# Optimization experiments

Hardware: AMD Instinct MI355X
Metric: run time of the kernel (lower is better)

## Reference

```python
import jax, jax.numpy as jnp
import numpy as np

NUM_BUCKETS = 64
MAX_DISTANCE = 50000.0


def setup_inputs() -> dict:
    R, I, N, E, H = 64, 512, 4, 256, 8
    key = jax.random.key(0)
    ks = jax.random.split(key, 12)
    p = lambda k, shape: (jax.random.normal(k, shape, dtype=jnp.float32) * 0.02)
    return {
        "x": jax.random.normal(ks[0], (R, I, N, E), dtype=jnp.float32),
        "distances": jax.random.randint(ks[1], (N, I, I), 0, 50000).astype(jnp.int32),
        "Wq": p(ks[2], (E, E)), "bq": jnp.zeros((E,), jnp.float32),
        "Wk": p(ks[3], (E, E)), "bk": jnp.zeros((E,), jnp.float32),
        "Wv": p(ks[4], (E, E)), "bv": jnp.zeros((E,), jnp.float32),
        "Wo": p(ks[5], (E, E)), "bo": jnp.zeros((E,), jnp.float32),
        "rel_emb": p(ks[6], (NUM_BUCKETS, H)),
    }


def reference(x, distances, Wq, bq, Wk, bk, Wv, bv, Wo, bo, rel_emb):
    R, I, N, E = x.shape
    H = rel_emb.shape[1]
    D = E // H
    # scaling = head_dim**-0.5 / sqrt(num_rows)
    scaling = (D ** -0.5) / np.sqrt(R)

    def proj(W, b):
        return (jnp.einsum('rine,fe->rinf', x, W) + b).reshape(R, I, N, H, D)

    q = proj(Wq, bq) * scaling
    k = proj(Wk, bk)
    v = proj(Wv, bv)

    # Row-summed attention logits: (H, N, I, J)
    attn_weights = jnp.einsum('rinhd,rjnhd->hnij', q, k)

    # T5-style relative position bias (buckets = linspace boundaries)
    buckets = jnp.linspace(0.0, MAX_DISTANCE, NUM_BUCKETS - 1)
    abs_dist = jnp.abs(distances).astype(jnp.float32)
    # torch.bucketize(right=False) == searchsorted side='left'
    bucket_idx = jnp.searchsorted(buckets, abs_dist, side='left')  # (N, I, J)
    bias = rel_emb[bucket_idx]                  # (N, I, J, H)
    attn_weights = attn_weights + jnp.transpose(bias, (3, 0, 1, 2))

    attn_probs = jax.nn.softmax(attn_weights, axis=-1)  # dropout p=0.0 -> identity

    context = jnp.einsum('hnij,rjnhd->rinhd', attn_probs, v).reshape(R, I, N, E)
    output = jnp.einsum('rine,fe->rinf', context, Wo) + bo
    return output, attn_probs
```

## Files before the change

kernel.cpp:

```cpp
#include <hip/hip_runtime.h>

typedef unsigned short u16;
typedef unsigned int u32;
typedef float f32x4 __attribute__((ext_vector_type(4)));
typedef short bf16x8 __attribute__((ext_vector_type(8)));
typedef unsigned short u16x8 __attribute__((ext_vector_type(8)));

#define SL 33554432u

__device__ __forceinline__ float bf2f(u16 u) {
  u32 v = ((u32)u) << 16;
  return __builtin_bit_cast(float, v);
}
__device__ __forceinline__ u16 f2bf(float f) {
  u32 i = __builtin_bit_cast(u32, f);
  i += 0x7fffu + ((i >> 16) & 1u);
  return (u16)(i >> 16);
}

#define GLDS16(g, l) __builtin_amdgcn_global_load_lds( \
    (const __attribute__((address_space(1))) void*)(g), \
    (__attribute__((address_space(3))) void*)(l), 16, 0, 0)

__device__ __forceinline__ void stage128(const u16* gbase, int ldk, u16* lds, int tid) {
  #pragma unroll
  for (int rep = 0; rep < 4; ++rep) {
    int c = tid + rep * 256;
    int row = c >> 3, slot = c & 7;
    const u16* g = gbase + (size_t)row * ldk + ((slot ^ (row & 7)) << 3);
    GLDS16(g, lds + c * 8);
  }
}

__device__ __forceinline__ void stage128_f32(const float* gbase, int ldk, u16* lds, int tid) {
  #pragma unroll
  for (int rep = 0; rep < 4; ++rep) {
    int c = tid + rep * 256;
    int row = c >> 3, slot = c & 7;
    const float* g = gbase + (size_t)row * ldk + ((slot ^ (row & 7)) << 3);
    float4 a = *(const float4*)g, b = *(const float4*)(g + 4);
    u16x8 o;
    o[0] = f2bf(a.x); o[1] = f2bf(a.y); o[2] = f2bf(a.z); o[3] = f2bf(a.w);
    o[4] = f2bf(b.x); o[5] = f2bf(b.y); o[6] = f2bf(b.z); o[7] = f2bf(b.w);
    *(u16x8*)(lds + c * 8) = o;
  }
}

__device__ __forceinline__ void mfma128(const u16* As, const u16* Bs, int lane,
                                        int wm0, int wn0, f32x4 acc[4][4]) {
  #pragma unroll
  for (int kk = 0; kk < 2; ++kk) {
    bf16x8 a[4], b[4];
    #pragma unroll
    for (int mi = 0; mi < 4; ++mi) {
      int r = wm0 + mi * 16 + (lane & 15);
      int c16 = (kk * 4 + (lane >> 4)) ^ (r & 7);
      a[mi] = *(const bf16x8*)(As + r * 64 + c16 * 8);
    }
    #pragma unroll
    for (int ni = 0; ni < 4; ++ni) {
      int r = wn0 + ni * 16 + (lane & 15);
      int c16 = (kk * 4 + (lane >> 4)) ^ (r & 7);
      b[ni] = *(const bf16x8*)(Bs + r * 64 + c16 * 8);
    }
    #pragma unroll
    for (int mi = 0; mi < 4; ++mi)
      #pragma unroll
      for (int ni = 0; ni < 4; ++ni)
        acc[mi][ni] = __builtin_amdgcn_mfma_f32_16x16x32_bf16(a[mi], b[ni], acc[mi][ni], 0, 0, 0);
  }
}

__device__ __forceinline__ void gemm_core(const u16* A, int ldkA, const u16* B, int ldkB,
                                          int NT, u16* As, u16* Bs,
                                          int tid, int lane, int wm0, int wn0,
                                          f32x4 acc[4][4]) {
  for (int t = 0; t < NT; ++t) {
    stage128(A + t * 64, ldkA, As, tid);
    stage128(B + t * 64, ldkB, Bs, tid);
    __syncthreads();
    mfma128(As, Bs, lane, wm0, wn0, acc);
    __syncthreads();
  }
}

__global__ __launch_bounds__(256) void k_castw(
    const float* __restrict__ Wq, const float* __restrict__ Wk,
    const float* __restrict__ Wv, const float* __restrict__ Wo,
    u16* __restrict__ Wb) {
  int idx = blockIdx.x * 256 + threadIdx.x;
  int w = idx >> 13, off = idx & 8191;
  const float* src = (w == 0) ? Wq : (w == 1) ? Wk : (w == 2) ? Wv : Wo;
  const float4* s = (const float4*)(src + (size_t)off * 8);
  float4 a = s[0], b = s[1];
  u16x8 o;
  o[0] = f2bf(a.x); o[1] = f2bf(a.y); o[2] = f2bf(a.z); o[3] = f2bf(a.w);
  o[4] = f2bf(b.x); o[5] = f2bf(b.y); o[6] = f2bf(b.z); o[7] = f2bf(b.w);
  *(u16x8*)(Wb + (size_t)w * 65536 + (size_t)off * 8) = o;
}

__global__ __launch_bounds__(256) void k_proj_mm(
    const float* __restrict__ x, const u16* __restrict__ Wb,
    const float* __restrict__ bq, const float* __restrict__ bk, const float* __restrict__ bv,
    u16* __restrict__ qt, u16* __restrict__ kt, u16* __restrict__ vt, float scaling) {
  __shared__ __align__(16) u16 As[128 * 64];
  __shared__ __align__(16) u16 Bs[128 * 64];
  const int tid = threadIdx.x, lane = tid & 63, wave = tid >> 6;
  const int wm0 = (wave >> 1) * 64, wn0 = (wave & 1) * 64;
  const int bid = blockIdx.x;
  const int sb = (bid & 7) * 768 + (bid >> 3);
  const int mt = sb / 6, g = sb % 6;
  const int m0 = mt * 128, n0 = (g & 1) * 128, w = g >> 1;

  f32x4 acc[4][4];
  #pragma unroll
  for (int mi = 0; mi < 4; ++mi)
    #pragma unroll
    for (int ni = 0; ni < 4; ++ni) acc[mi][ni] = (f32x4){0.f, 0.f, 0.f, 0.f};

  const float* Ax = x + (size_t)m0 * 256;
  const u16* Bw = Wb + w * 65536 + (size_t)n0 * 256;
  for (int t = 0; t < 4; ++t) {
    stage128_f32(Ax + t * 64, 256, As, tid);
    stage128(Bw + t * 64, 256, Bs, tid);
    __syncthreads();
    mfma128(As, Bs, lane, wm0, wn0, acc);
    __syncthreads();
  }

  const float* bias = (w == 0) ? bq : (w == 1) ? bk : bv;
  u16* dst = (w == 0) ? qt : (w == 1) ? kt : vt;
  const float sc = (w == 0) ? scaling : 1.0f;

  #pragma unroll
  for (int mi = 0; mi < 4; ++mi)
    #pragma unroll
    for (int ni = 0; ni < 4; ++ni) {
      int f = n0 + wn0 + ni * 16 + (lane & 15);
      int h = f >> 5, d = f & 31;
      float bb = bias[f];
      #pragma unroll
      for (int q = 0; q < 4; ++q) {
        int m = m0 + wm0 + mi * 16 + (lane >> 4) * 4 + q;
        int n = m & 3, i = (m >> 2) & 511, r = m >> 11;
        size_t o = ((size_t)((n * 8 + h) * 512 + i)) * 2048 + r * 32 + d;
        dst[o] = f2bf((acc[mi][ni][q] + bb) * sc);
      }
    }
}

__global__ __launch_bounds__(256) void k_attn_mm(
    const u16* __restrict__ qt, const u16* __restrict__ kt, u16* __restrict__ lgt) {
  __shared__ __align__(16) u16 As[128 * 64];
  __shared__ __align__(16) u16 Bs[128 * 64];
  const int tid = threadIdx.x, lane = tid & 63, wave = tid >> 6;
  const int wm0 = (wave >> 1) * 64, wn0 = (wave & 1) * 64;
  const int bid = blockIdx.x;
  const int sb = (bid & 7) * 64 + (bid >> 3);
  const int nh = sb >> 4, tt = sb & 15;
  const int m0 = (tt >> 2) * 128, n0 = (tt & 3) * 128;

  f32x4 acc[4][4];
  #pragma unroll
  for (int mi = 0; mi < 4; ++mi)
    #pragma unroll
    for (int ni = 0; ni < 4; ++ni) acc[mi][ni] = (f32x4){0.f, 0.f, 0.f, 0.f};

  const size_t base = (size_t)nh * 512 * 2048;
  gemm_core(qt + base + (size_t)m0 * 2048, 2048, kt + base + (size_t)n0 * 2048, 2048,
            32, As, Bs, tid, lane, wm0, wn0, acc);

  #pragma unroll
  for (int mi = 0; mi < 4; ++mi)
    #pragma unroll
    for (int ni = 0; ni < 4; ++ni) {
      int col = n0 + wn0 + ni * 16 + (lane & 15);
      #pragma unroll
      for (int q = 0; q < 4; ++q) {
        int row = m0 + wm0 + mi * 16 + (lane >> 4) * 4 + q;
        lgt[(size_t)nh * 262144 + (size_t)row * 512 + col] = f2bf(acc[mi][ni][q]);
      }
    }
}

__global__ __launch_bounds__(256) void k_softmax(
    const u16* __restrict__ lgt, const int* __restrict__ dist, const float* __restrict__ rel,
    float* __restrict__ probs, u16* __restrict__ pbf) {
  const int t = threadIdx.x;
  const int lane = t & 63, wv = t >> 6;
  const int b = blockIdx.x;
  const int i = b & 511, n = b >> 9;

  const int* dr = dist + ((size_t)n * 512 + i) * 512 + lane * 8;
  int4 dA = *(const int4*)dr, dB = *(const int4*)(dr + 4);
  int dd[8] = {dA.x, dA.y, dA.z, dA.w, dB.x, dB.y, dB.z, dB.w};
  int u[8];
  #pragma unroll
  for (int j = 0; j < 8; ++j) {
    int v = dd[j] < 0 ? -dd[j] : dd[j];
    int q = (62 * v + 49999) / 50000; if (q > 63) q = 63;
    u[j] = q;
  }

  #pragma unroll
  for (int hh = 0; hh < 2; ++hh) {
    const int h = wv * 2 + hh;
    const int nh = n * 8 + h;
    const u16* lr = lgt + ((size_t)nh * 512 + i) * 512 + lane * 8;
    u16x8 L = *(const u16x8*)lr;
    float vj[8];
    float mx = -1e30f;
    #pragma unroll
    for (int j = 0; j < 8; ++j) {
      vj[j] = bf2f(L[j]) + rel[u[j] * 8 + h];
      mx = fmaxf(mx, vj[j]);
    }
    #pragma unroll
    for (int off = 32; off; off >>= 1) mx = fmaxf(mx, __shfl_xor(mx, off));
    float s = 0.f;
    #pragma unroll
    for (int j = 0; j < 8; ++j) { vj[j] = __expf(vj[j] - mx); s += vj[j]; }
    #pragma unroll
    for (int off = 32; off; off >>= 1) s += __shfl_xor(s, off);
    float inv = 1.0f / s;
    float4 pa, pb;
    pa.x = vj[0]*inv; pa.y = vj[1]*inv; pa.z = vj[2]*inv; pa.w = vj[3]*inv;
    pb.x = vj[4]*inv; pb.y = vj[5]*inv; pb.z = vj[6]*inv; pb.w = vj[7]*inv;
    size_t po = ((size_t)(h * 4 + n) * 512 + i) * 512 + lane * 8;
    *(float4*)(probs + po) = pa;
    *(float4*)(probs + po + 4) = pb;
    u16x8 pc;
    pc[0]=f2bf(pa.x); pc[1]=f2bf(pa.y); pc[2]=f2bf(pa.z); pc[3]=f2bf(pa.w);
    pc[4]=f2bf(pb.x); pc[5]=f2bf(pb.y); pc[6]=f2bf(pb.z); pc[7]=f2bf(pb.w);
    size_t pq = ((size_t)nh * 512 + i) * 512 + lane * 8;
    *(u16x8*)(pbf + pq) = pc;
  }
}

__global__ __launch_bounds__(256) void k_vtrans(const u16* __restrict__ vt, u16* __restrict__ vtt) {
  __shared__ u16 ts[64][72];
  const int b = blockIdx.x;
  const int ct_ = b & 31, it = (b >> 5) & 7, nh = b >> 8;
  const int i0 = it * 64, c0 = ct_ * 64;
  const int t = threadIdx.x;
  #pragma unroll
  for (int rep = 0; rep < 2; ++rep) {
    int c = t + rep * 256;
    int r = c >> 3, q = c & 7;
    u16x8 v = *(const u16x8*)(vt + ((size_t)nh * 512 + i0 + r) * 2048 + c0 + q * 8);
    #pragma unroll
    for (int j = 0; j < 8; ++j) ts[r][q * 8 + j] = v[j];
  }
  __syncthreads();
  #pragma unroll
  for (int rep = 0; rep < 2; ++rep) {
    int c = t + rep * 256;
    int rr = c >> 3, q = c & 7;
    u16x8 o;
    #pragma unroll
    for (int j = 0; j < 8; ++j) o[j] = ts[q * 8 + j][rr];
    *(u16x8*)(vtt + ((size_t)nh * 2048 + c0 + rr) * 512 + i0 + q * 8) = o;
  }
}

__global__ __launch_bounds__(256) void k_ctx_mm(
    const u16* __restrict__ vtt, const u16* __restrict__ pbf, u16* __restrict__ ctT) {
  __shared__ __align__(16) u16 As[128 * 64];
  __shared__ __align__(16) u16 Bs[128 * 64];
  const int tid = threadIdx.x, lane = tid & 63, wave = tid >> 6;
  const int wm0 = (wave >> 1) * 64, wn0 = (wave & 1) * 64;
  const int bid = blockIdx.x;
  const int sb = (bid & 7) * 256 + (bid >> 3);
  const int nh = sb >> 6, tt = sb & 63;
  const int m0 = (tt >> 2) * 128, n0 = (tt & 3) * 128;

  f32x4 acc[4][4];
  #pragma unroll
  for (int mi = 0; mi < 4; ++mi)
    #pragma unroll
    for (int ni = 0; ni < 4; ++ni) acc[mi][ni] = (f32x4){0.f, 0.f, 0.f, 0.f};

  gemm_core(vtt + (size_t)nh * 1048576 + (size_t)m0 * 512, 512,
            pbf + (size_t)nh * 262144 + (size_t)n0 * 512, 512,
            8, As, Bs, tid, lane, wm0, wn0, acc);

  #pragma unroll
  for (int mi = 0; mi < 4; ++mi)
    #pragma unroll
    for (int ni = 0; ni < 4; ++ni) {
      int col = n0 + wn0 + ni * 16 + (lane & 15);
      #pragma unroll
      for (int q = 0; q < 4; ++q) {
        int row = m0 + wm0 + mi * 16 + (lane >> 4) * 4 + q;
        ctT[(size_t)nh * 1048576 + (size_t)row * 512 + col] = f2bf(acc[mi][ni][q]);
      }
    }
}

__global__ __launch_bounds__(256) void k_ctrans(const u16* __restrict__ ctT, u16* __restrict__ ct) {
  __shared__ u16 ts[32][520];
  const int b = blockIdx.x;
  const int r = b & 63, nh = b >> 6;
  const int n = nh >> 3, h = nh & 7;
  const int t = threadIdx.x;
  #pragma unroll
  for (int rep = 0; rep < 8; ++rep) {
    int c = t + rep * 256;
    int d = c >> 6, q = c & 63;
    u16x8 v = *(const u16x8*)(ctT + ((size_t)nh * 2048 + r * 32 + d) * 512 + q * 8);
    #pragma unroll
    for (int j = 0; j < 8; ++j) ts[d][q * 8 + j] = v[j];
  }
  __syncthreads();
  #pragma unroll
  for (int rep = 0; rep < 8; ++rep) {
    int c = t + rep * 256;
    int i = c >> 2, q = c & 3;
    u16x8 o;
    #pragma unroll
    for (int j = 0; j < 8; ++j) o[j] = ts[q * 8 + j][i];
    *(u16x8*)(ct + ((size_t)((r * 512 + i) * 4 + n)) * 256 + h * 32 + q * 8) = o;
  }
}

__global__ __launch_bounds__(256) void k_oproj_mm(
    const u16* __restrict__ ct, const u16* __restrict__ Wob,
    const float* __restrict__ bo, float* __restrict__ out) {
  __shared__ __align__(16) u16 As[128 * 64];
  __shared__ __align__(16) u16 Bs[128 * 64];
  const int tid = threadIdx.x, lane = tid & 63, wave = tid >> 6;
  const int wm0 = (wave >> 1) * 64, wn0 = (wave & 1) * 64;
  const int bid = blockIdx.x;
  const int sb = (bid & 7) * 256 + (bid >> 3);
  const int m0 = (sb >> 1) * 128, n0 = (sb & 1) * 128;

  f32x4 acc[4][4];
  #pragma unroll
  for (int mi = 0; mi < 4; ++mi)
    #pragma unroll
    for (int ni = 0; ni < 4; ++ni) acc[mi][ni] = (f32x4){0.f, 0.f, 0.f, 0.f};

  gemm_core(ct + (size_t)m0 * 256, 256, Wob + (size_t)n0 * 256, 256,
            4, As, Bs, tid, lane, wm0, wn0, acc);

  #pragma unroll
  for (int mi = 0; mi < 4; ++mi)
    #pragma unroll
    for (int ni = 0; ni < 4; ++ni) {
      int col = n0 + wn0 + ni * 16 + (lane & 15);
      float bb = bo[col];
      #pragma unroll
      for (int q = 0; q < 4; ++q) {
        int row = m0 + wm0 + mi * 16 + (lane >> 4) * 4 + q;
        out[(size_t)row * 256 + col] = acc[mi][ni][q] + bb;
      }
    }
}

extern "C" void kernel_launch(void* const* d_in, const int* in_sizes, int n_in,
                              void* d_out, int out_size, void* d_ws, size_t ws_size,
                              hipStream_t stream) {
  const float* x  = (const float*)d_in[0];
  const int* dist = (const int*)d_in[1];
  const float* Wq = (const float*)d_in[2];
  const float* bq = (const float*)d_in[3];
  const float* Wk = (const float*)d_in[4];
  const float* bk = (const float*)d_in[5];
  const float* Wv = (const float*)d_in[6];
  const float* bv = (const float*)d_in[7];
  const float* Wo = (const float*)d_in[8];
  const float* bo = (const float*)d_in[9];
  const float* rel = (const float*)d_in[10];
  float* out = (float*)d_out;
  float* probs = out + (size_t)SL;

  u16* ws = (u16*)d_ws;
  u16* lgt = ws;
  u16* qt  = ws + (size_t)SL;
  u16* kt  = ws + (size_t)2 * SL;
  u16* vt  = ws + (size_t)3 * SL;
  u16* pbf = qt;
  u16* vtt = kt;
  u16* ctT = vt;
  u16* ctb = lgt;
  u16* Wb  = ws + (size_t)4 * SL;

  const float scaling = 0.022097086912079608f;

  k_castw  <<<128, 256, 0, stream>>>(Wq, Wk, Wv, Wo, Wb);
  k_proj_mm<<<6144, 256, 0, stream>>>(x, Wb, bq, bk, bv, qt, kt, vt, scaling);
  k_attn_mm<<<512, 256, 0, stream>>>(qt, kt, lgt);
  k_softmax<<<2048, 256, 0, stream>>>(lgt, dist, rel, probs, pbf);
  k_vtrans <<<8192, 256, 0, stream>>>(vt, vtt);
  k_ctx_mm <<<2048, 256, 0, stream>>>(vtt, pbf, ctT);
  k_ctrans <<<2048, 256, 0, stream>>>(ctT, ctb);
  k_oproj_mm<<<2048, 256, 0, stream>>>(ctb, Wb + 196608, bo, out);
}
```

Before: 402.0 us.

## Fuse V and context transposes into GEMM epilogues; precast x to bf16

Removes the standalone k_vtrans and k_ctrans kernels. The projection and context GEMM epilogues now stage their tiles through LDS and write directly in the transposed layouts, using vectorized 16-byte stores instead of scattered 2-byte stores. x is converted to bf16 once by a separate cast kernel, so the projection GEMM can stage it with global_load_lds instead of per-thread fp32 loads and converts. This adds an extra full pass over x and a bf16 copy of it, and makes the epilogues more complex with possible LDS bank conflicts on the transposed V writes.

Result: faster. 374.8 us (-6.8%).

```diff
diff --git a/kernel.cpp b/kernel.cpp
--- a/kernel.cpp
+++ b/kernel.cpp
@@ -29,20 +29,6 @@
     int row = c >> 3, slot = c & 7;
     const u16* g = gbase + (size_t)row * ldk + ((slot ^ (row & 7)) << 3);
     GLDS16(g, lds + c * 8);
-  }
-}
-
-__device__ __forceinline__ void stage128_f32(const float* gbase, int ldk, u16* lds, int tid) {
-  #pragma unroll
-  for (int rep = 0; rep < 4; ++rep) {
-    int c = tid + rep * 256;
-    int row = c >> 3, slot = c & 7;
-    const float* g = gbase + (size_t)row * ldk + ((slot ^ (row & 7)) << 3);
-    float4 a = *(const float4*)g, b = *(const float4*)(g + 4);
-    u16x8 o;
-    o[0] = f2bf(a.x); o[1] = f2bf(a.y); o[2] = f2bf(a.z); o[3] = f2bf(a.w);
-    o[4] = f2bf(b.x); o[5] = f2bf(b.y); o[6] = f2bf(b.z); o[7] = f2bf(b.w);
-    *(u16x8*)(lds + c * 8) = o;
   }
 }
 
@@ -82,6 +68,17 @@
     mfma128(As, Bs, lane, wm0, wn0, acc);
     __syncthreads();
   }
+}
+
+__global__ __launch_bounds__(256) void k_castx(const float* __restrict__ src,
+                                               u16* __restrict__ dst) {
+  int idx = blockIdx.x * 256 + threadIdx.x;
+  const float4* s = (const float4*)src;
+  float4 a = s[(size_t)idx * 2], b = s[(size_t)idx * 2 + 1];
+  u16x8 o;
+  o[0] = f2bf(a.x); o[1] = f2bf(a.y); o[2] = f2bf(a.z); o[3] = f2bf(a.w);
+  o[4] = f2bf(b.x); o[5] = f2bf(b.y); o[6] = f2bf(b.z); o[7] = f2bf(b.w);
+  *(u16x8*)(dst + (size_t)idx * 8) = o;
 }
 
 __global__ __launch_bounds__(256) void k_castw(
@@ -100,17 +97,22 @@
 }
 
 __global__ __launch_bounds__(256) void k_proj_mm(
-    const float* __restrict__ x, const u16* __restrict__ Wb,
+    const u16* __restrict__ xb, const u16* __restrict__ Wb,
     const float* __restrict__ bq, const float* __restrict__ bk, const float* __restrict__ bv,
-    u16* __restrict__ qt, u16* __restrict__ kt, u16* __restrict__ vt, float scaling) {
-  __shared__ __align__(16) u16 As[128 * 64];
-  __shared__ __align__(16) u16 Bs[128 * 64];
+    u16* __restrict__ qt, u16* __restrict__ kt, u16* __restrict__ vtt, float scaling) {
+  __shared__ __align__(16) u16 lds[17408];
+  u16* As = lds;
+  u16* Bs = lds + 8192;
+  u16* ts = lds;
   const int tid = threadIdx.x, lane = tid & 63, wave = tid >> 6;
   const int wm0 = (wave >> 1) * 64, wn0 = (wave & 1) * 64;
   const int bid = blockIdx.x;
   const int sb = (bid & 7) * 768 + (bid >> 3);
   const int mt = sb / 6, g = sb % 6;
   const int m0 = mt * 128, n0 = (g & 1) * 128, w = g >> 1;
+  const int h0 = n0 >> 5;
+  const int r = mt >> 4;
+  const int i0 = (mt * 32) & 511;
 
   f32x4 acc[4][4];
   #pragma unroll
@@ -118,35 +120,68 @@
     #pragma unroll
     for (int ni = 0; ni < 4; ++ni) acc[mi][ni] = (f32x4){0.f, 0.f, 0.f, 0.f};
 
-  const float* Ax = x + (size_t)m0 * 256;
-  const u16* Bw = Wb + w * 65536 + (size_t)n0 * 256;
-  for (int t = 0; t < 4; ++t) {
-    stage128_f32(Ax + t * 64, 256, As, tid);
-    stage128(Bw + t * 64, 256, Bs, tid);
+  gemm_core(xb + (size_t)m0 * 256, 256, Wb + w * 65536 + (size_t)n0 * 256, 256,
+            4, As, Bs, tid, lane, wm0, wn0, acc);
+
+  const float* bias = (w == 0) ? bq : (w == 1) ? bk : bv;
+  const float sc = (w == 0) ? scaling : 1.0f;
+
+  if (w < 2) {
+    #pragma unroll
+    for (int mi = 0; mi < 4; ++mi)
+      #pragma unroll
+      for (int ni = 0; ni < 4; ++ni) {
+        int f_l = wn0 + ni * 16 + (lane & 15);
+        float bb = bias[n0 + f_l];
+        #pragma unroll
+        for (int q = 0; q < 4; ++q) {
+          int m_l = wm0 + mi * 16 + (lane >> 4) * 4 + q;
+          ts[m_l * 136 + f_l] = f2bf((acc[mi][ni][q] + bb) * sc);
+        }
+      }
     __syncthreads();
-    mfma128(As, Bs, lane, wm0, wn0, acc);
+    u16* dst = (w == 0) ? qt : kt;
+    #pragma unroll
+    for (int cc = 0; cc < 2; ++cc) {
+      int ch = tid + cc * 256;
+      int i_l = ch & 31, hh = (ch >> 5) & 3, n = ch >> 7;
+      const u16* src = ts + (i_l * 4 + n) * 136 + hh * 32;
+      size_t o = ((size_t)((n * 8 + h0 + hh) * 512) + i0 + i_l) * 2048 + r * 32;
+      #pragma unroll
+      for (int j = 0; j < 4; ++j)
+        *(u16x8*)(dst + o + j * 8) = *(const u16x8*)(src + j * 8);
+    }
+  } else {
+    #pragma unroll
+    for (int mi = 0; mi < 4; ++mi)
+      #pragma unroll
+      for (int ni = 0; ni < 4; ++ni) {
+        int f_l = wn0 + ni * 16 + (lane & 15);
+        float bb = bias[n0 + f_l];
+        #pragma unroll
+        for (int q = 0; q < 4; ++q) {
+          int m_l = wm0 + mi * 16 + (lane >> 4) * 4 + q;
+          ts[f_l * 136 + m_l] = f2bf(acc[mi][ni][q] + bb);
+        }
+      }
     __syncthreads();
-  }
-
-  const float* bias = (w == 0) ? bq : (w == 1) ? bk : bv;
-  u16* dst = (w == 0) ? qt : (w == 1) ? kt : vt;
-  const float sc = (w == 0) ? scaling : 1.0f;
-
-  #pragma unroll
-  for (int mi = 0; mi < 4; ++mi)
-    #pragma unroll
-    for (int ni = 0; ni < 4; ++ni) {
-      int f = n0 + wn0 + ni * 16 + (lane & 15);
-      int h = f >> 5, d = f & 31;
-      float bb = bias[f];
-      #pragma unroll
-      for (int q = 0; q < 4; ++q) {
-        int m = m0 + wm0 + mi * 16 + (lane >> 4) * 4 + q;
-        int n = m & 3, i = (m >> 2) & 511, r = m >> 11;
-        size_t o = ((size_t)((n * 8 + h) * 512 + i)) * 2048 + r * 32 + d;
-        dst[o] = f2bf((acc[mi][ni][q] + bb) * sc);
-      }
-    }
+    #pragma unroll
+    for (int cc = 0; cc < 2; ++cc) {
+      int ch = tid + cc * 256;
+      int d = ch & 31, hh = (ch >> 5) & 3, n = ch >> 7;
+      const u16* src = ts + (hh * 32 + d) * 136;
+      u16x8 tmp[4];
+      #pragma unroll
+      for (int j = 0; j < 4; ++j)
+        #pragma unroll
+        for (int e = 0; e < 8; ++e)
+          tmp[j][e] = src[(j * 8 + e) * 4 + n];
+      size_t o = ((size_t)(n * 8 + h0 + hh) * 2048 + r * 32 + d) * 512 + i0;
+      #pragma unroll
+      for (int j = 0; j < 4; ++j)
+        *(u16x8*)(vtt + o + j * 8) = tmp[j];
+    }
+  }
 }
 
 __global__ __launch_bounds__(256) void k_attn_mm(
@@ -237,42 +272,19 @@
   }
 }
 
-__global__ __launch_bounds__(256) void k_vtrans(const u16* __restrict__ vt, u16* __restrict__ vtt) {
-  __shared__ u16 ts[64][72];
-  const int b = blockIdx.x;
-  const int ct_ = b & 31, it = (b >> 5) & 7, nh = b >> 8;
-  const int i0 = it * 64, c0 = ct_ * 64;
-  const int t = threadIdx.x;
-  #pragma unroll
-  for (int rep = 0; rep < 2; ++rep) {
-    int c = t + rep * 256;
-    int r = c >> 3, q = c & 7;
-    u16x8 v = *(const u16x8*)(vt + ((size_t)nh * 512 + i0 + r) * 2048 + c0 + q * 8);
-    #pragma unroll
-    for (int j = 0; j < 8; ++j) ts[r][q * 8 + j] = v[j];
-  }
-  __syncthreads();
-  #pragma unroll
-  for (int rep = 0; rep < 2; ++rep) {
-    int c = t + rep * 256;
-    int rr = c >> 3, q = c & 7;
-    u16x8 o;
-    #pragma unroll
-    for (int j = 0; j < 8; ++j) o[j] = ts[q * 8 + j][rr];
-    *(u16x8*)(vtt + ((size_t)nh * 2048 + c0 + rr) * 512 + i0 + q * 8) = o;
-  }
-}
-
 __global__ __launch_bounds__(256) void k_ctx_mm(
-    const u16* __restrict__ vtt, const u16* __restrict__ pbf, u16* __restrict__ ctT) {
-  __shared__ __align__(16) u16 As[128 * 64];
-  __shared__ __align__(16) u16 Bs[128 * 64];
+    const u16* __restrict__ vtt, const u16* __restrict__ pbf, u16* __restrict__ ct) {
+  __shared__ __align__(16) u16 lds[17408];
+  u16* As = lds;
+  u16* Bs = lds + 8192;
+  u16* ts = lds;
   const int tid = threadIdx.x, lane = tid & 63, wave = tid >> 6;
   const int wm0 = (wave >> 1) * 64, wn0 = (wave & 1) * 64;
   const int bid = blockIdx.x;
   const int sb = (bid & 7) * 256 + (bid >> 3);
   const int nh = sb >> 6, tt = sb & 63;
   const int m0 = (tt >> 2) * 128, n0 = (tt & 3) * 128;
+  const int n = nh >> 3, h = nh & 7;
 
   f32x4 acc[4][4];
   #pragma unroll
@@ -288,38 +300,24 @@
   for (int mi = 0; mi < 4; ++mi)
     #pragma unroll
     for (int ni = 0; ni < 4; ++ni) {
-      int col = n0 + wn0 + ni * 16 + (lane & 15);
+      int i_l = wn0 + ni * 16 + (lane & 15);
       #pragma unroll
       for (int q = 0; q < 4; ++q) {
-        int row = m0 + wm0 + mi * 16 + (lane >> 4) * 4 + q;
-        ctT[(size_t)nh * 1048576 + (size_t)row * 512 + col] = f2bf(acc[mi][ni][q]);
-      }
-    }
-}
-
-__global__ __launch_bounds__(256) void k_ctrans(const u16* __restrict__ ctT, u16* __restrict__ ct) {
-  __shared__ u16 ts[32][520];
-  const int b = blockIdx.x;
-  const int r = b & 63, nh = b >> 6;
-  const int n = nh >> 3, h = nh & 7;
-  const int t = threadIdx.x;
-  #pragma unroll
-  for (int rep = 0; rep < 8; ++rep) {
-    int c = t + rep * 256;
-    int d = c >> 6, q = c & 63;
-    u16x8 v = *(const u16x8*)(ctT + ((size_t)nh * 2048 + r * 32 + d) * 512 + q * 8);
-    #pragma unroll
-    for (int j = 0; j < 8; ++j) ts[d][q * 8 + j] = v[j];
-  }
+        int c_l = wm0 + mi * 16 + (lane >> 4) * 4 + q;
+        ts[i_l * 136 + c_l] = f2bf(acc[mi][ni][q]);
+      }
+    }
   __syncthreads();
   #pragma unroll
-  for (int rep = 0; rep < 8; ++rep) {
-    int c = t + rep * 256;
-    int i = c >> 2, q = c & 3;
-    u16x8 o;
-    #pragma unroll
-    for (int j = 0; j < 8; ++j) o[j] = ts[q * 8 + j][i];
-    *(u16x8*)(ct + ((size_t)((r * 512 + i) * 4 + n)) * 256 + h * 32 + q * 8) = o;
+  for (int cc = 0; cc < 2; ++cc) {
+    int ch = tid + cc * 256;
+    int i_l = ch & 127, r_l = ch >> 7;
+    const u16* src = ts + i_l * 136 + r_l * 32;
+    int rr = (m0 >> 5) + r_l;
+    size_t o = ((size_t)((rr * 512 + n0 + i_l) * 4 + n)) * 256 + h * 32;
+    #pragma unroll
+    for (int j = 0; j < 4; ++j)
+      *(u16x8*)(ct + o + j * 8) = *(const u16x8*)(src + j * 8);
   }
 }
 
@@ -375,24 +373,22 @@
   float* probs = out + (size_t)SL;
 
   u16* ws = (u16*)d_ws;
-  u16* lgt = ws;
+  u16* xb  = ws;
   u16* qt  = ws + (size_t)SL;
   u16* kt  = ws + (size_t)2 * SL;
-  u16* vt  = ws + (size_t)3 * SL;
+  u16* vtt = ws + (size_t)3 * SL;
+  u16* lgt = xb;
   u16* pbf = qt;
-  u16* vtt = kt;
-  u16* ctT = vt;
-  u16* ctb = lgt;
+  u16* ctb = kt;
   u16* Wb  = ws + (size_t)4 * SL;
 
   const float scaling = 0.022097086912079608f;
 
+  k_castx  <<<16384, 256, 0, stream>>>(x, xb);
   k_castw  <<<128, 256, 0, stream>>>(Wq, Wk, Wv, Wo, Wb);
-  k_proj_mm<<<6144, 256, 0, stream>>>(x, Wb, bq, bk, bv, qt, kt, vt, scaling);
+  k_proj_mm<<<6144, 256, 0, stream>>>(xb, Wb, bq, bk, bv, qt, kt, vtt, scaling);
   k_attn_mm<<<512, 256, 0, stream>>>(qt, kt, lgt);
   k_softmax<<<2048, 256, 0, stream>>>(lgt, dist, rel, probs, pbf);
-  k_vtrans <<<8192, 256, 0, stream>>>(vt, vtt);
-  k_ctx_mm <<<2048, 256, 0, stream>>>(vtt, pbf, ctT);
-  k_ctrans <<<2048, 256, 0, stream>>>(ctT, ctb);
+  k_ctx_mm <<<2048, 256, 0, stream>>>(vtt, pbf, ctb);
   k_oproj_mm<<<2048, 256, 0, stream>>>(ctb, Wb + 196608, bo, out);
 }
```

## Fuse context transpose into ctx GEMM epilogue and pre-cast x to bf16

Applied to the files above, without the earlier changes.

The separate k_ctrans kernel is removed: k_ctx_mm now stages its output tile through padded LDS and writes the context directly in the (r,i,n,e) layout that the output projection consumes, avoiding a full intermediate write and read. Separately, x is cast to bf16 once by a new k_castx kernel, so k_proj_mm can use async global-to-LDS loads through gemm_core instead of converting fp32 inside each block, where each x tile was read and converted six times. The cast adds an extra pass over x plus a kernel launch, and the LDS transpose adds a sync in the ctx epilogue.

After: 337.7 us. 16.0% less time.

```diff
diff --git a/kernel.cpp b/kernel.cpp
--- a/kernel.cpp
+++ b/kernel.cpp
@@ -29,20 +29,6 @@
     int row = c >> 3, slot = c & 7;
     const u16* g = gbase + (size_t)row * ldk + ((slot ^ (row & 7)) << 3);
     GLDS16(g, lds + c * 8);
-  }
-}
-
-__device__ __forceinline__ void stage128_f32(const float* gbase, int ldk, u16* lds, int tid) {
-  #pragma unroll
-  for (int rep = 0; rep < 4; ++rep) {
-    int c = tid + rep * 256;
-    int row = c >> 3, slot = c & 7;
-    const float* g = gbase + (size_t)row * ldk + ((slot ^ (row & 7)) << 3);
-    float4 a = *(const float4*)g, b = *(const float4*)(g + 4);
-    u16x8 o;
-    o[0] = f2bf(a.x); o[1] = f2bf(a.y); o[2] = f2bf(a.z); o[3] = f2bf(a.w);
-    o[4] = f2bf(b.x); o[5] = f2bf(b.y); o[6] = f2bf(b.z); o[7] = f2bf(b.w);
-    *(u16x8*)(lds + c * 8) = o;
   }
 }
 
@@ -82,6 +68,17 @@
     mfma128(As, Bs, lane, wm0, wn0, acc);
     __syncthreads();
   }
+}
+
+__global__ __launch_bounds__(256) void k_castx(const float* __restrict__ src,
+                                               u16* __restrict__ dst) {
+  int idx = blockIdx.x * 256 + threadIdx.x;
+  const float4* s = (const float4*)src;
+  float4 a = s[(size_t)idx * 2], b = s[(size_t)idx * 2 + 1];
+  u16x8 o;
+  o[0] = f2bf(a.x); o[1] = f2bf(a.y); o[2] = f2bf(a.z); o[3] = f2bf(a.w);
+  o[4] = f2bf(b.x); o[5] = f2bf(b.y); o[6] = f2bf(b.z); o[7] = f2bf(b.w);
+  *(u16x8*)(dst + (size_t)idx * 8) = o;
 }
 
 __global__ __launch_bounds__(256) void k_castw(
@@ -100,7 +97,7 @@
 }
 
 __global__ __launch_bounds__(256) void k_proj_mm(
-    const float* __restrict__ x, const u16* __restrict__ Wb,
+    const u16* __restrict__ xb, const u16* __restrict__ Wb,
     const float* __restrict__ bq, const float* __restrict__ bk, const float* __restrict__ bv,
     u16* __restrict__ qt, u16* __restrict__ kt, u16* __restrict__ vt, float scaling) {
   __shared__ __align__(16) u16 As[128 * 64];
@@ -118,15 +115,8 @@
     #pragma unroll
     for (int ni = 0; ni < 4; ++ni) acc[mi][ni] = (f32x4){0.f, 0.f, 0.f, 0.f};
 
-  const float* Ax = x + (size_t)m0 * 256;
-  const u16* Bw = Wb + w * 65536 + (size_t)n0 * 256;
-  for (int t = 0; t < 4; ++t) {
-    stage128_f32(Ax + t * 64, 256, As, tid);
-    stage128(Bw + t * 64, 256, Bs, tid);
-    __syncthreads();
-    mfma128(As, Bs, lane, wm0, wn0, acc);
-    __syncthreads();
-  }
+  gemm_core(xb + (size_t)m0 * 256, 256, Wb + w * 65536 + (size_t)n0 * 256, 256,
+            4, As, Bs, tid, lane, wm0, wn0, acc);
 
   const float* bias = (w == 0) ? bq : (w == 1) ? bk : bv;
   u16* dst = (w == 0) ? qt : (w == 1) ? kt : vt;
@@ -264,15 +254,18 @@
 }
 
 __global__ __launch_bounds__(256) void k_ctx_mm(
-    const u16* __restrict__ vtt, const u16* __restrict__ pbf, u16* __restrict__ ctT) {
-  __shared__ __align__(16) u16 As[128 * 64];
-  __shared__ __align__(16) u16 Bs[128 * 64];
+    const u16* __restrict__ vtt, const u16* __restrict__ pbf, u16* __restrict__ ct) {
+  __shared__ __align__(16) u16 lds[16640];
+  u16* As = lds;
+  u16* Bs = lds + 8192;
+  u16* ts = lds;
   const int tid = threadIdx.x, lane = tid & 63, wave = tid >> 6;
   const int wm0 = (wave >> 1) * 64, wn0 = (wave & 1) * 64;
   const int bid = blockIdx.x;
   const int sb = (bid & 7) * 256 + (bid >> 3);
   const int nh = sb >> 6, tt = sb & 63;
   const int m0 = (tt >> 2) * 128, n0 = (tt & 3) * 128;
+  const int n = nh >> 3, h = nh & 7;
 
   f32x4 acc[4][4];
   #pragma unroll
@@ -288,38 +281,24 @@
   for (int mi = 0; mi < 4; ++mi)
     #pragma unroll
     for (int ni = 0; ni < 4; ++ni) {
-      int col = n0 + wn0 + ni * 16 + (lane & 15);
+      int i_l = wn0 + ni * 16 + (lane & 15);
       #pragma unroll
       for (int q = 0; q < 4; ++q) {
-        int row = m0 + wm0 + mi * 16 + (lane >> 4) * 4 + q;
-        ctT[(size_t)nh * 1048576 + (size_t)row * 512 + col] = f2bf(acc[mi][ni][q]);
+        int c_l = wm0 + mi * 16 + (lane >> 4) * 4 + q;
+        ts[i_l * 130 + c_l] = f2bf(acc[mi][ni][q]);
       }
     }
-}
-
-__global__ __launch_bounds__(256) void k_ctrans(const u16* __restrict__ ctT, u16* __restrict__ ct) {
-  __shared__ u16 ts[32][520];
-  const int b = blockIdx.x;
-  const int r = b & 63, nh = b >> 6;
-  const int n = nh >> 3, h = nh & 7;
-  const int t = threadIdx.x;
-  #pragma unroll
-  for (int rep = 0; rep < 8; ++rep) {
-    int c = t + rep * 256;
-    int d = c >> 6, q = c & 63;
-    u16x8 v = *(const u16x8*)(ctT + ((size_t)nh * 2048 + r * 32 + d) * 512 + q * 8);
-    #pragma unroll
-    for (int j = 0; j < 8; ++j) ts[d][q * 8 + j] = v[j];
-  }
   __syncthreads();
   #pragma unroll
-  for (int rep = 0; rep < 8; ++rep) {
-    int c = t + rep * 256;
-    int i = c >> 2, q = c & 3;
-    u16x8 o;
-    #pragma unroll
-    for (int j = 0; j < 8; ++j) o[j] = ts[q * 8 + j][i];
-    *(u16x8*)(ct + ((size_t)((r * 512 + i) * 4 + n)) * 256 + h * 32 + q * 8) = o;
+  for (int cc = 0; cc < 2; ++cc) {
+    int ch = tid + cc * 256;
+    int i_l = ch & 127, r_l = ch >> 7;
+    const u16* src = ts + i_l * 130 + r_l * 32;
+    int rr = (m0 >> 5) + r_l;
+    size_t o = ((size_t)((rr * 512 + n0 + i_l) * 4 + n)) * 256 + h * 32;
+    #pragma unroll
+    for (int j = 0; j < 4; ++j)
+      *(u16x8*)(ct + o + j * 8) = *(const u16x8*)(src + j * 8);
   }
 }
 
@@ -375,24 +354,24 @@
   float* probs = out + (size_t)SL;
 
   u16* ws = (u16*)d_ws;
-  u16* lgt = ws;
+  u16* xb  = ws;
   u16* qt  = ws + (size_t)SL;
   u16* kt  = ws + (size_t)2 * SL;
   u16* vt  = ws + (size_t)3 * SL;
+  u16* lgt = xb;
   u16* pbf = qt;
   u16* vtt = kt;
-  u16* ctT = vt;
-  u16* ctb = lgt;
+  u16* ctb = xb;
   u16* Wb  = ws + (size_t)4 * SL;
 
   const float scaling = 0.022097086912079608f;
 
+  k_castx  <<<16384, 256, 0, stream>>>(x, xb);
   k_castw  <<<128, 256, 0, stream>>>(Wq, Wk, Wv, Wo, Wb);
-  k_proj_mm<<<6144, 256, 0, stream>>>(x, Wb, bq, bk, bv, qt, kt, vt, scaling);
+  k_proj_mm<<<6144, 256, 0, stream>>>(xb, Wb, bq, bk, bv, qt, kt, vt, scaling);
   k_attn_mm<<<512, 256, 0, stream>>>(qt, kt, lgt);
   k_softmax<<<2048, 256, 0, stream>>>(lgt, dist, rel, probs, pbf);
   k_vtrans <<<8192, 256, 0, stream>>>(vt, vtt);
-  k_ctx_mm <<<2048, 256, 0, stream>>>(vtt, pbf, ctT);
-  k_ctrans <<<2048, 256, 0, stream>>>(ctT, ctb);
+  k_ctx_mm <<<2048, 256, 0, stream>>>(vtt, pbf, ctb);
   k_oproj_mm<<<2048, 256, 0, stream>>>(ctb, Wb + 196608, bo, out);
 }
```
